# Performance work log

Hardware: AMD Instinct MI355X
Metric: run time of the kernel (lower is better)

Reference implementation:

```python
import jax, jax.numpy as jnp
import numpy as np

D_MODEL = 1024
N_HEAD = 16
HEAD_DIM = D_MODEL // N_HEAD


def setup_inputs() -> dict:
    key = jax.random.key(0)
    ks = jax.random.split(key, 9)
    B, S, D = 2, 2048, D_MODEL
    s = 1.0 / np.sqrt(D)
    return {
        "x": jax.random.normal(ks[0], (B, S, D), dtype=jnp.float32),
        "Wq": jax.random.normal(ks[1], (D, D), dtype=jnp.float32) * s,
        "bq": jnp.zeros((D,), dtype=jnp.float32),
        "Wk": jax.random.normal(ks[2], (D, D), dtype=jnp.float32) * s,
        "bk": jnp.zeros((D,), dtype=jnp.float32),
        "Wv": jax.random.normal(ks[3], (D, D), dtype=jnp.float32) * s,
        "bv": jnp.zeros((D,), dtype=jnp.float32),
        "Wo": jax.random.normal(ks[4], (D, D), dtype=jnp.float32) * s,
        "bo": jnp.zeros((D,), dtype=jnp.float32),
    }


def _split_heads(t):
    B, S, D = t.shape
    return t.reshape(B, S, N_HEAD, HEAD_DIM).transpose(0, 2, 1, 3)  # [B,H,S,d]


def reference(x, Wq, bq, Wk, bk, Wv, bv, Wo, bo):
    B, S, D = x.shape
    q = _split_heads(x @ Wq + bq)
    k = _split_heads(x @ Wk + bk)
    v = _split_heads(x @ Wv + bv)
    present = jnp.stack((k, v))  # [2,B,H,S,d]
    # NOTE: module scales by sqrt(d_model), not sqrt(head_dim)
    scores = jnp.einsum("bhqd,bhkd->bhqk", q, k) / jnp.sqrt(jnp.float32(D_MODEL))
    causal = jnp.tril(jnp.ones((S, S), dtype=bool))
    scores = jnp.where(causal, scores, -jnp.inf)
    probs = jax.nn.softmax(scores, axis=-1)
    attn = jnp.einsum("bhqk,bhkd->bhqd", probs, v)
    attn = attn.transpose(0, 2, 1, 3).reshape(B, S, D)
    out = attn @ Wo + bo
    return out, present
```

## Files before the change

kernel.cpp:

```cpp
#include <hip/hip_runtime.h>
#include <hip/hip_bf16.h>

typedef __attribute__((ext_vector_type(8))) short short8;
typedef __attribute__((ext_vector_type(4))) short short4v;
typedef __attribute__((ext_vector_type(4))) float f32x4;

#define S_LEN 2048
#define DM 1024
#define NH 16
#define HD 64

__device__ __forceinline__ short f2b(float f) {
    __hip_bfloat16 h = __float2bfloat16(f);
    return *reinterpret_cast<short*>(&h);
}

__global__ void k_convert_x(const float* __restrict__ x, short* __restrict__ xb) {
    size_t i = ((size_t)blockIdx.x * blockDim.x + threadIdx.x) * 4;
    f32x4 v = *reinterpret_cast<const f32x4*>(x + i);
    short4v o;
    for (int e = 0; e < 4; e++) o[e] = f2b(v[e]);
    *reinterpret_cast<short4v*>(xb + i) = o;
}

__global__ void k_transpose_w4(const float* __restrict__ W0, const float* __restrict__ W1,
                               const float* __restrict__ W2, const float* __restrict__ W3,
                               short* __restrict__ T0, short* __restrict__ T1,
                               short* __restrict__ T2, short* __restrict__ T3) {
    __shared__ float tile[32][33];
    const int z = blockIdx.z;
    const float* W = (z == 0) ? W0 : (z == 1) ? W1 : (z == 2) ? W2 : W3;
    short* Wt = (z == 0) ? T0 : (z == 1) ? T1 : (z == 2) ? T2 : T3;
    int tx = threadIdx.x, ty = threadIdx.y;
    int nb = blockIdx.x * 32, kb = blockIdx.y * 32;
    for (int i = 0; i < 4; i++)
        tile[ty + i * 8][tx] = W[(size_t)(kb + ty + i * 8) * DM + nb + tx];
    __syncthreads();
    for (int i = 0; i < 4; i++)
        Wt[(size_t)(nb + ty + i * 8) * DM + kb + tx] = f2b(tile[tx][ty + i * 8]);
}

__global__ __launch_bounds__(256) void k_gemm_qkv(
    const short* __restrict__ xb,
    const short* __restrict__ Wqt, const short* __restrict__ Wkt, const short* __restrict__ Wvt,
    const float* __restrict__ bq, const float* __restrict__ bk, const float* __restrict__ bv,
    short* __restrict__ Qb, short* __restrict__ Kfrag, short* __restrict__ Vfrag,
    float* __restrict__ pK, float* __restrict__ pV)
{
    __shared__ alignas(16) short As[128][72];
    __shared__ alignas(16) short Bs[128][72];
    const int z = blockIdx.z;
    const short* Wt  = (z == 0) ? Wqt : (z == 1) ? Wkt : Wvt;
    const float* bias = (z == 0) ? bq : (z == 1) ? bk : bv;
    const int t = threadIdx.x;
    const int brow = blockIdx.y * 128, bcol = blockIdx.x * 128;
    const int w = t >> 6, l = t & 63;
    const int wr = w >> 1, wc = w & 1;
    const int lr = l & 15, lg = l >> 4;
    f32x4 acc[4][4];
    for (int m = 0; m < 4; m++) for (int n = 0; n < 4; n++) acc[m][n] = (f32x4)0.0f;

    for (int k0 = 0; k0 < DM; k0 += 64) {
        __syncthreads();
        for (int i = 0; i < 4; i++) {
            int idx = i * 256 + t;
            int r = idx >> 3, c8 = (idx & 7) * 8;
            *reinterpret_cast<short8*>(&As[r][c8]) =
                *reinterpret_cast<const short8*>(&xb[(size_t)(brow + r) * DM + k0 + c8]);
            *reinterpret_cast<short8*>(&Bs[r][c8]) =
                *reinterpret_cast<const short8*>(&Wt[(size_t)(bcol + r) * DM + k0 + c8]);
        }
        __syncthreads();
        for (int ks = 0; ks < 2; ks++) {
            short8 a[4], bb[4];
            const int kk = ks * 32 + lg * 8;
            for (int m = 0; m < 4; m++)
                a[m] = *reinterpret_cast<const short8*>(&As[wr * 64 + m * 16 + lr][kk]);
            for (int n = 0; n < 4; n++)
                bb[n] = *reinterpret_cast<const short8*>(&Bs[wc * 64 + n * 16 + lr][kk]);
            for (int m = 0; m < 4; m++)
                for (int n = 0; n < 4; n++)
                    acc[m][n] = __builtin_amdgcn_mfma_f32_16x16x32_bf16(a[m], bb[n], acc[m][n], 0, 0, 0);
        }
    }
    for (int m = 0; m < 4; m++)
        for (int n = 0; n < 4; n++) {
            int row = brow + wr * 64 + m * 16 + lg * 4;
            int col = bcol + wc * 64 + n * 16 + lr;
            float bv_ = bias[col];
            int b_ = row >> 11, sI0 = row & 2047, hI = col >> 6, dh = col & 63;
            if (z == 0) {
                for (int r = 0; r < 4; r++) {
                    float v = acc[m][n][r] + bv_;
                    Qb[(size_t)(row + r) * DM + col] = f2b(v * 0.0450842200575152f);
                }
            } else if (z == 1) {
                for (int r = 0; r < 4; r++) {
                    float v = acc[m][n][r] + bv_;
                    int sI = sI0 + r;
                    pK[(((size_t)(b_ * NH + hI)) * S_LEN + sI) * HD + dh] = v;
                    int j = sI >> 6, kk = sI & 63;
                    int cg = ((kk >> 4) & 2) | ((kk >> 2) & 1);
                    int lrA = ((kk >> 3) & 3) * 4 + (kk & 3);
                    int lane = lrA + ((dh >> 3) & 3) * 16;
                    int ks = dh >> 5, e = dh & 7;
                    Kfrag[((((size_t)(b_ * NH + hI) * 32 + j) * 2 + ks) * 4 + cg) * 512
                          + lane * 8 + e] = f2b(v);
                }
            } else {
                int j = sI0 >> 6, ks = (sI0 >> 5) & 1;
                int dg = dh >> 4;
                int lane = (dh & 15) + ((sI0 >> 3) & 3) * 16;
                int e0 = sI0 & 7;
                short4v tv;
                for (int r = 0; r < 4; r++) {
                    float v = acc[m][n][r] + bv_;
                    pV[(((size_t)(b_ * NH + hI)) * S_LEN + (sI0 + r)) * HD + dh] = v;
                    tv[r] = f2b(v);
                }
                *reinterpret_cast<short4v*>(
                    &Vfrag[((((size_t)(b_ * NH + hI) * 32 + j) * 2 + ks) * 4 + dg) * 512
                           + lane * 8 + e0]) = tv;
            }
        }
}

__global__ __launch_bounds__(256) void k_gemm_o(
    const short* __restrict__ Ab, const short* __restrict__ Wot,
    const float* __restrict__ bo, float* __restrict__ out)
{
    __shared__ alignas(16) short As[128][72];
    __shared__ alignas(16) short Bs[128][72];
    const int t = threadIdx.x;
    const int brow = blockIdx.y * 128, bcol = blockIdx.x * 128;
    const int w = t >> 6, l = t & 63;
    const int wr = w >> 1, wc = w & 1;
    const int lr = l & 15, lg = l >> 4;
    f32x4 acc[4][4];
    for (int m = 0; m < 4; m++) for (int n = 0; n < 4; n++) acc[m][n] = (f32x4)0.0f;

    for (int k0 = 0; k0 < DM; k0 += 64) {
        __syncthreads();
        for (int i = 0; i < 4; i++) {
            int idx = i * 256 + t;
            int r = idx >> 3, c8 = (idx & 7) * 8;
            *reinterpret_cast<short8*>(&As[r][c8]) =
                *reinterpret_cast<const short8*>(&Ab[(size_t)(brow + r) * DM + k0 + c8]);
            *reinterpret_cast<short8*>(&Bs[r][c8]) =
                *reinterpret_cast<const short8*>(&Wot[(size_t)(bcol + r) * DM + k0 + c8]);
        }
        __syncthreads();
        for (int ks = 0; ks < 2; ks++) {
            short8 a[4], bb[4];
            const int kk = ks * 32 + lg * 8;
            for (int m = 0; m < 4; m++)
                a[m] = *reinterpret_cast<const short8*>(&As[wr * 64 + m * 16 + lr][kk]);
            for (int n = 0; n < 4; n++)
                bb[n] = *reinterpret_cast<const short8*>(&Bs[wc * 64 + n * 16 + lr][kk]);
            for (int m = 0; m < 4; m++)
                for (int n = 0; n < 4; n++)
                    acc[m][n] = __builtin_amdgcn_mfma_f32_16x16x32_bf16(a[m], bb[n], acc[m][n], 0, 0, 0);
        }
    }
    for (int m = 0; m < 4; m++)
        for (int n = 0; n < 4; n++) {
            int row = brow + wr * 64 + m * 16 + lg * 4;
            int col = bcol + wc * 64 + n * 16 + lr;
            float bv_ = bo[col];
            for (int r = 0; r < 4; r++)
                out[(size_t)(row + r) * DM + col] = acc[m][n][r] + bv_;
        }
}

__global__ __launch_bounds__(64) void k_attn(
    const short* __restrict__ Qb, const short* __restrict__ Kfrag,
    const short* __restrict__ Vfrag, short* __restrict__ Ab)
{
    const int bid = blockIdx.x;
    const int orig = (bid & 7) * 256 + (bid >> 3);
    const int bh = orig >> 6, rp = orig & 63;
    const int h = bh & 15, b = bh >> 4;
    const int l = threadIdx.x;
    const int lr = l & 15, lg = l >> 4;
    const size_t base = (size_t)b * S_LEN * DM + (size_t)h * HD;
    const short* Qp = Qb + base;
    const short* Kbh = Kfrag + (size_t)bh * 32 * 4096;
    const short* Vbh = Vfrag + (size_t)bh * 32 * 4096;
    short* Ap = Ab + base;

    for (int phase = 0; phase < 2; ++phase) {
        const int strip = phase ? 127 - rp : rp;
        const int jmax = strip >> 2;
        const int qrow = strip * 16 + lr;
        short8 qf0 = *reinterpret_cast<const short8*>(Qp + (size_t)qrow * DM + lg * 8);
        short8 qf1 = *reinterpret_cast<const short8*>(Qp + (size_t)qrow * DM + 32 + lg * 8);
        f32x4 o[4];
#pragma unroll
        for (int dg = 0; dg < 4; dg++) o[dg] = (f32x4)0.0f;
        float mrun = -INFINITY, lrun = 0.0f;

        const short* kp = Kbh + l * 8;
        const short* vp = Vbh + l * 8;
        short8 kc[2][4], vc[2][4];
#pragma unroll
        for (int ks = 0; ks < 2; ks++)
#pragma unroll
            for (int cg = 0; cg < 4; cg++) {
                kc[ks][cg] = *reinterpret_cast<const short8*>(kp + (ks * 4 + cg) * 512);
                vc[ks][cg] = *reinterpret_cast<const short8*>(vp + (ks * 4 + cg) * 512);
            }

        for (int j = 0; j <= jmax; ++j) {
            f32x4 s[4];
#pragma unroll
            for (int cg = 0; cg < 4; cg++) s[cg] = (f32x4)0.0f;
#pragma unroll
            for (int ks = 0; ks < 2; ks++) {
                const short8 qf = ks ? qf1 : qf0;
#pragma unroll
                for (int cg = 0; cg < 4; cg++)
                    s[cg] = __builtin_amdgcn_mfma_f32_16x16x32_bf16(kc[ks][cg], qf, s[cg], 0, 0, 0);
            }
            if (j < jmax) {
                kp += 4096;
#pragma unroll
                for (int ks = 0; ks < 2; ks++)
#pragma unroll
                    for (int cg = 0; cg < 4; cg++)
                        kc[ks][cg] = *reinterpret_cast<const short8*>(kp + (ks * 4 + cg) * 512);
            }
            if (j == jmax) {
#pragma unroll
                for (int cg = 0; cg < 4; cg++)
#pragma unroll
                    for (int r = 0; r < 4; r++) {
                        int n = ((cg >> 1) << 5) + (lg << 3) + ((cg & 1) << 2) + r;
                        if (j * 64 + n > qrow) s[cg][r] = -INFINITY;
                    }
            }
            float mx0 = fmaxf(fmaxf(s[0][0], s[0][1]), fmaxf(s[0][2], s[0][3]));
            float mx1 = fmaxf(fmaxf(s[1][0], s[1][1]), fmaxf(s[1][2], s[1][3]));
            float mx2 = fmaxf(fmaxf(s[2][0], s[2][1]), fmaxf(s[2][2], s[2][3]));
            float mx3 = fmaxf(fmaxf(s[3][0], s[3][1]), fmaxf(s[3][2], s[3][3]));
            float vmax = fmaxf(fmaxf(mx0, mx1), fmaxf(mx2, mx3));
            vmax = fmaxf(vmax, __shfl_xor(vmax, 16));
            vmax = fmaxf(vmax, __shfl_xor(vmax, 32));
            if (!__all(vmax - mrun <= 8.0f)) {
                float mn = fmaxf(mrun, vmax);
                float scl = exp2f(mrun - mn);
                mrun = mn; lrun *= scl;
#pragma unroll
                for (int dg = 0; dg < 4; dg++)
#pragma unroll
                    for (int r = 0; r < 4; r++) o[dg][r] *= scl;
            }
            float rs = 0.0f;
#pragma unroll
            for (int cg = 0; cg < 4; cg++)
#pragma unroll
                for (int r = 0; r < 4; r++) {
                    float p = exp2f(s[cg][r] - mrun);
                    s[cg][r] = p;
                    rs += p;
                }
            rs += __shfl_xor(rs, 16);
            rs += __shfl_xor(rs, 32);
            lrun += rs;
            short8 pf0, pf1;
#pragma unroll
            for (int r = 0; r < 4; r++) {
                pf0[r] = f2b(s[0][r]); pf0[4 + r] = f2b(s[1][r]);
                pf1[r] = f2b(s[2][r]); pf1[4 + r] = f2b(s[3][r]);
            }
#pragma unroll
            for (int ks = 0; ks < 2; ks++) {
                const short8 pf = ks ? pf1 : pf0;
#pragma unroll
                for (int dg = 0; dg < 4; dg++)
                    o[dg] = __builtin_amdgcn_mfma_f32_16x16x32_bf16(vc[ks][dg], pf, o[dg], 0, 0, 0);
            }
            if (j < jmax) {
                vp += 4096;
#pragma unroll
                for (int ks = 0; ks < 2; ks++)
#pragma unroll
                    for (int cg = 0; cg < 4; cg++)
                        vc[ks][cg] = *reinterpret_cast<const short8*>(vp + (ks * 4 + cg) * 512);
            }
        }
        float rinv = 1.0f / lrun;
#pragma unroll
        for (int dg = 0; dg < 4; dg++) {
            short4v ov;
#pragma unroll
            for (int r = 0; r < 4; r++) ov[r] = f2b(o[dg][r] * rinv);
            *reinterpret_cast<short4v*>(Ap + (size_t)qrow * DM + dg * 16 + lg * 4) = ov;
        }
    }
}

extern "C" void kernel_launch(void* const* d_in, const int* in_sizes, int n_in,
                              void* d_out, int out_size, void* d_ws, size_t ws_size,
                              hipStream_t stream) {
    const float* x  = (const float*)d_in[0];
    const float* Wq = (const float*)d_in[1];
    const float* bq = (const float*)d_in[2];
    const float* Wk = (const float*)d_in[3];
    const float* bk = (const float*)d_in[4];
    const float* Wv = (const float*)d_in[5];
    const float* bv = (const float*)d_in[6];
    const float* Wo = (const float*)d_in[7];
    const float* bo = (const float*)d_in[8];

    float* out = (float*)d_out;
    float* presentK = out + (size_t)4194304;
    float* presentV = presentK + (size_t)4194304;

    char* ws = (char*)d_ws;
    short* xb    = (short*)(ws);
    short* Wqt   = (short*)(ws + ((size_t)8  << 20));
    short* Wkt   = (short*)(ws + ((size_t)10 << 20));
    short* Wvt   = (short*)(ws + ((size_t)12 << 20));
    short* Wot   = (short*)(ws + ((size_t)14 << 20));
    short* Qb    = (short*)(ws + ((size_t)16 << 20));
    short* Kfrag = (short*)(ws + ((size_t)24 << 20));
    short* Vfrag = (short*)(ws + ((size_t)32 << 20));
    short* Ab    = (short*)(ws + ((size_t)40 << 20));

    k_convert_x<<<dim3(4096), dim3(256), 0, stream>>>(x, xb);
    k_transpose_w4<<<dim3(32, 32, 4), dim3(32, 8), 0, stream>>>(
        Wq, Wk, Wv, Wo, Wqt, Wkt, Wvt, Wot);
    k_gemm_qkv<<<dim3(8, 32, 3), dim3(256), 0, stream>>>(
        xb, Wqt, Wkt, Wvt, bq, bk, bv, Qb, Kfrag, Vfrag, presentK, presentV);
    k_attn<<<dim3(2048), dim3(64), 0, stream>>>(Qb, Kfrag, Vfrag, Ab);
    k_gemm_o<<<dim3(8, 32), dim3(256), 0, stream>>>(Ab, Wot, bo, out);
}
```

Baseline: 140.9 us.

## Process two query strips per wave sharing K/V fragments, two waves per block

Each wave now handles two adjacent 16-row query strips (A and B) against the same K/V fragment loads, halving K/V global traffic per query row. The former sequential two-phase causal balancing becomes two waves per block, each taking a mirrored strip pair, and the grid halves to 1024 blocks of 128 threads. In exchange, register pressure roughly doubles for accumulators and scores, which may reduce occupancy, and there are fewer blocks in flight.

```diff
diff --git a/kernel.cpp b/kernel.cpp
--- a/kernel.cpp
+++ b/kernel.cpp
@@ -172,15 +172,15 @@
         }
 }
 
-__global__ __launch_bounds__(64) void k_attn(
+__global__ __launch_bounds__(128) void k_attn(
     const short* __restrict__ Qb, const short* __restrict__ Kfrag,
     const short* __restrict__ Vfrag, short* __restrict__ Ab)
 {
     const int bid = blockIdx.x;
-    const int orig = (bid & 7) * 256 + (bid >> 3);
-    const int bh = orig >> 6, rp = orig & 63;
+    const int orig = (bid & 7) * 128 + (bid >> 3);
+    const int bh = orig >> 5, kidx = orig & 31;
     const int h = bh & 15, b = bh >> 4;
-    const int l = threadIdx.x;
+    const int w = threadIdx.x >> 6, l = threadIdx.x & 63;
     const int lr = l & 15, lg = l >> 4;
     const size_t base = (size_t)b * S_LEN * DM + (size_t)h * HD;
     const short* Qp = Qb + base;
@@ -188,114 +188,166 @@
     const short* Vbh = Vfrag + (size_t)bh * 32 * 4096;
     short* Ap = Ab + base;
 
-    for (int phase = 0; phase < 2; ++phase) {
-        const int strip = phase ? 127 - rp : rp;
-        const int jmax = strip >> 2;
-        const int qrow = strip * 16 + lr;
-        short8 qf0 = *reinterpret_cast<const short8*>(Qp + (size_t)qrow * DM + lg * 8);
-        short8 qf1 = *reinterpret_cast<const short8*>(Qp + (size_t)qrow * DM + 32 + lg * 8);
-        f32x4 o[4];
-#pragma unroll
-        for (int dg = 0; dg < 4; dg++) o[dg] = (f32x4)0.0f;
-        float mrun = -INFINITY, lrun = 0.0f;
-
-        const short* kp = Kbh + l * 8;
-        const short* vp = Vbh + l * 8;
-        short8 kc[2][4], vc[2][4];
-#pragma unroll
-        for (int ks = 0; ks < 2; ks++)
+    const int kj = w ? 63 - kidx : kidx;
+    const int jmax = kj >> 1;
+    const int qrowA = (2 * kj) * 16 + lr;
+    const int qrowB = (2 * kj + 1) * 16 + lr;
+
+    short8 qfA0 = *reinterpret_cast<const short8*>(Qp + (size_t)qrowA * DM + lg * 8);
+    short8 qfA1 = *reinterpret_cast<const short8*>(Qp + (size_t)qrowA * DM + 32 + lg * 8);
+    short8 qfB0 = *reinterpret_cast<const short8*>(Qp + (size_t)qrowB * DM + lg * 8);
+    short8 qfB1 = *reinterpret_cast<const short8*>(Qp + (size_t)qrowB * DM + 32 + lg * 8);
+    f32x4 oA[4], oB[4];
+#pragma unroll
+    for (int dg = 0; dg < 4; dg++) { oA[dg] = (f32x4)0.0f; oB[dg] = (f32x4)0.0f; }
+    float mrunA = -INFINITY, lrunA = 0.0f;
+    float mrunB = -INFINITY, lrunB = 0.0f;
+
+    const short* kp = Kbh + l * 8;
+    const short* vp = Vbh + l * 8;
+    short8 kc[2][4], vc[2][4];
+#pragma unroll
+    for (int ks = 0; ks < 2; ks++)
+#pragma unroll
+        for (int cg = 0; cg < 4; cg++) {
+            kc[ks][cg] = *reinterpret_cast<const short8*>(kp + (ks * 4 + cg) * 512);
+            vc[ks][cg] = *reinterpret_cast<const short8*>(vp + (ks * 4 + cg) * 512);
+        }
+
+    for (int j = 0; j <= jmax; ++j) {
+        f32x4 sA[4], sB[4];
+#pragma unroll
+        for (int cg = 0; cg < 4; cg++) { sA[cg] = (f32x4)0.0f; sB[cg] = (f32x4)0.0f; }
+#pragma unroll
+        for (int ks = 0; ks < 2; ks++) {
+            const short8 qfa = ks ? qfA1 : qfA0;
+            const short8 qfb = ks ? qfB1 : qfB0;
 #pragma unroll
             for (int cg = 0; cg < 4; cg++) {
-                kc[ks][cg] = *reinterpret_cast<const short8*>(kp + (ks * 4 + cg) * 512);
-                vc[ks][cg] = *reinterpret_cast<const short8*>(vp + (ks * 4 + cg) * 512);
-            }
-
-        for (int j = 0; j <= jmax; ++j) {
-            f32x4 s[4];
-#pragma unroll
-            for (int cg = 0; cg < 4; cg++) s[cg] = (f32x4)0.0f;
-#pragma unroll
-            for (int ks = 0; ks < 2; ks++) {
-                const short8 qf = ks ? qf1 : qf0;
+                sA[cg] = __builtin_amdgcn_mfma_f32_16x16x32_bf16(kc[ks][cg], qfa, sA[cg], 0, 0, 0);
+                sB[cg] = __builtin_amdgcn_mfma_f32_16x16x32_bf16(kc[ks][cg], qfb, sB[cg], 0, 0, 0);
+            }
+        }
+        if (j < jmax) {
+            kp += 4096;
+#pragma unroll
+            for (int ks = 0; ks < 2; ks++)
 #pragma unroll
                 for (int cg = 0; cg < 4; cg++)
-                    s[cg] = __builtin_amdgcn_mfma_f32_16x16x32_bf16(kc[ks][cg], qf, s[cg], 0, 0, 0);
-            }
-            if (j < jmax) {
-                kp += 4096;
-#pragma unroll
-                for (int ks = 0; ks < 2; ks++)
-#pragma unroll
-                    for (int cg = 0; cg < 4; cg++)
-                        kc[ks][cg] = *reinterpret_cast<const short8*>(kp + (ks * 4 + cg) * 512);
-            }
-            if (j == jmax) {
-#pragma unroll
-                for (int cg = 0; cg < 4; cg++)
-#pragma unroll
-                    for (int r = 0; r < 4; r++) {
-                        int n = ((cg >> 1) << 5) + (lg << 3) + ((cg & 1) << 2) + r;
-                        if (j * 64 + n > qrow) s[cg][r] = -INFINITY;
-                    }
-            }
-            float mx0 = fmaxf(fmaxf(s[0][0], s[0][1]), fmaxf(s[0][2], s[0][3]));
-            float mx1 = fmaxf(fmaxf(s[1][0], s[1][1]), fmaxf(s[1][2], s[1][3]));
-            float mx2 = fmaxf(fmaxf(s[2][0], s[2][1]), fmaxf(s[2][2], s[2][3]));
-            float mx3 = fmaxf(fmaxf(s[3][0], s[3][1]), fmaxf(s[3][2], s[3][3]));
+                    kc[ks][cg] = *reinterpret_cast<const short8*>(kp + (ks * 4 + cg) * 512);
+        }
+        if (j == jmax) {
+#pragma unroll
+            for (int cg = 0; cg < 4; cg++)
+#pragma unroll
+                for (int r = 0; r < 4; r++) {
+                    int n = ((cg >> 1) << 5) + (lg << 3) + ((cg & 1) << 2) + r;
+                    if (j * 64 + n > qrowA) sA[cg][r] = -INFINITY;
+                    if (j * 64 + n > qrowB) sB[cg][r] = -INFINITY;
+                }
+        }
+        short8 pfA0, pfA1;
+        {
+            float mx0 = fmaxf(fmaxf(sA[0][0], sA[0][1]), fmaxf(sA[0][2], sA[0][3]));
+            float mx1 = fmaxf(fmaxf(sA[1][0], sA[1][1]), fmaxf(sA[1][2], sA[1][3]));
+            float mx2 = fmaxf(fmaxf(sA[2][0], sA[2][1]), fmaxf(sA[2][2], sA[2][3]));
+            float mx3 = fmaxf(fmaxf(sA[3][0], sA[3][1]), fmaxf(sA[3][2], sA[3][3]));
             float vmax = fmaxf(fmaxf(mx0, mx1), fmaxf(mx2, mx3));
             vmax = fmaxf(vmax, __shfl_xor(vmax, 16));
             vmax = fmaxf(vmax, __shfl_xor(vmax, 32));
-            if (!__all(vmax - mrun <= 8.0f)) {
-                float mn = fmaxf(mrun, vmax);
-                float scl = exp2f(mrun - mn);
-                mrun = mn; lrun *= scl;
+            if (!__all(vmax - mrunA <= 8.0f)) {
+                float mn = fmaxf(mrunA, vmax);
+                float scl = exp2f(mrunA - mn);
+                mrunA = mn; lrunA *= scl;
 #pragma unroll
                 for (int dg = 0; dg < 4; dg++)
 #pragma unroll
-                    for (int r = 0; r < 4; r++) o[dg][r] *= scl;
+                    for (int r = 0; r < 4; r++) oA[dg][r] *= scl;
             }
             float rs = 0.0f;
 #pragma unroll
             for (int cg = 0; cg < 4; cg++)
 #pragma unroll
                 for (int r = 0; r < 4; r++) {
-                    float p = exp2f(s[cg][r] - mrun);
-                    s[cg][r] = p;
+                    float p = exp2f(sA[cg][r] - mrunA);
+                    sA[cg][r] = p;
                     rs += p;
                 }
             rs += __shfl_xor(rs, 16);
             rs += __shfl_xor(rs, 32);
-            lrun += rs;
-            short8 pf0, pf1;
+            lrunA += rs;
 #pragma unroll
             for (int r = 0; r < 4; r++) {
-                pf0[r] = f2b(s[0][r]); pf0[4 + r] = f2b(s[1][r]);
-                pf1[r] = f2b(s[2][r]); pf1[4 + r] = f2b(s[3][r]);
-            }
-#pragma unroll
-            for (int ks = 0; ks < 2; ks++) {
-                const short8 pf = ks ? pf1 : pf0;
+                pfA0[r] = f2b(sA[0][r]); pfA0[4 + r] = f2b(sA[1][r]);
+                pfA1[r] = f2b(sA[2][r]); pfA1[4 + r] = f2b(sA[3][r]);
+            }
+        }
+        short8 pfB0, pfB1;
+        {
+            float mx0 = fmaxf(fmaxf(sB[0][0], sB[0][1]), fmaxf(sB[0][2], sB[0][3]));
+            float mx1 = fmaxf(fmaxf(sB[1][0], sB[1][1]), fmaxf(sB[1][2], sB[1][3]));
+            float mx2 = fmaxf(fmaxf(sB[2][0], sB[2][1]), fmaxf(sB[2][2], sB[2][3]));
+            float mx3 = fmaxf(fmaxf(sB[3][0], sB[3][1]), fmaxf(sB[3][2], sB[3][3]));
+            float vmax = fmaxf(fmaxf(mx0, mx1), fmaxf(mx2, mx3));
+            vmax = fmaxf(vmax, __shfl_xor(vmax, 16));
+            vmax = fmaxf(vmax, __shfl_xor(vmax, 32));
+            if (!__all(vmax - mrunB <= 8.0f)) {
+                float mn = fmaxf(mrunB, vmax);
+                float scl = exp2f(mrunB - mn);
+                mrunB = mn; lrunB *= scl;
 #pragma unroll
                 for (int dg = 0; dg < 4; dg++)
-                    o[dg] = __builtin_amdgcn_mfma_f32_16x16x32_bf16(vc[ks][dg], pf, o[dg], 0, 0, 0);
-            }
-            if (j < jmax) {
-                vp += 4096;
-#pragma unroll
-                for (int ks = 0; ks < 2; ks++)
-#pragma unroll
-                    for (int cg = 0; cg < 4; cg++)
-                        vc[ks][cg] = *reinterpret_cast<const short8*>(vp + (ks * 4 + cg) * 512);
-            }
-        }
-        float rinv = 1.0f / lrun;
-#pragma unroll
-        for (int dg = 0; dg < 4; dg++) {
-            short4v ov;
-#pragma unroll
-            for (int r = 0; r < 4; r++) ov[r] = f2b(o[dg][r] * rinv);
-            *reinterpret_cast<short4v*>(Ap + (size_t)qrow * DM + dg * 16 + lg * 4) = ov;
-        }
+#pragma unroll
+                    for (int r = 0; r < 4; r++) oB[dg][r] *= scl;
+            }
+            float rs = 0.0f;
+#pragma unroll
+            for (int cg = 0; cg < 4; cg++)
+#pragma unroll
+                for (int r = 0; r < 4; r++) {
+                    float p = exp2f(sB[cg][r] - mrunB);
+                    sB[cg][r] = p;
+                    rs += p;
+                }
+            rs += __shfl_xor(rs, 16);
+            rs += __shfl_xor(rs, 32);
+            lrunB += rs;
+#pragma unroll
+            for (int r = 0; r < 4; r++) {
+                pfB0[r] = f2b(sB[0][r]); pfB0[4 + r] = f2b(sB[1][r]);
+                pfB1[r] = f2b(sB[2][r]); pfB1[4 + r] = f2b(sB[3][r]);
+            }
+        }
+#pragma unroll
+        for (int ks = 0; ks < 2; ks++) {
+            const short8 pfa = ks ? pfA1 : pfA0;
+            const short8 pfb = ks ? pfB1 : pfB0;
+#pragma unroll
+            for (int dg = 0; dg < 4; dg++) {
+                oA[dg] = __builtin_amdgcn_mfma_f32_16x16x32_bf16(vc[ks][dg], pfa, oA[dg], 0, 0, 0);
+                oB[dg] = __builtin_amdgcn_mfma_f32_16x16x32_bf16(vc[ks][dg], pfb, oB[dg], 0, 0, 0);
+            }
+        }
+        if (j < jmax) {
+            vp += 4096;
+#pragma unroll
+            for (int ks = 0; ks < 2; ks++)
+#pragma unroll
+                for (int cg = 0; cg < 4; cg++)
+                    vc[ks][cg] = *reinterpret_cast<const short8*>(vp + (ks * 4 + cg) * 512);
+        }
+    }
+    float rinvA = 1.0f / lrunA, rinvB = 1.0f / lrunB;
+#pragma unroll
+    for (int dg = 0; dg < 4; dg++) {
+        short4v ovA, ovB;
+#pragma unroll
+        for (int r = 0; r < 4; r++) {
+            ovA[r] = f2b(oA[dg][r] * rinvA);
+            ovB[r] = f2b(oB[dg][r] * rinvB);
+        }
+        *reinterpret_cast<short4v*>(Ap + (size_t)qrowA * DM + dg * 16 + lg * 4) = ovA;
+        *reinterpret_cast<short4v*>(Ap + (size_t)qrowB * DM + dg * 16 + lg * 4) = ovB;
     }
 }
 
@@ -332,6 +384,6 @@
         Wq, Wk, Wv, Wo, Wqt, Wkt, Wvt, Wot);
     k_gemm_qkv<<<dim3(8, 32, 3), dim3(256), 0, stream>>>(
         xb, Wqt, Wkt, Wvt, bq, bk, bv, Qb, Kfrag, Vfrag, presentK, presentV);
-    k_attn<<<dim3(2048), dim3(64), 0, stream>>>(Qb, Kfrag, Vfrag, Ab);
+    k_attn<<<dim3(1024), dim3(128), 0, stream>>>(Qb, Kfrag, Vfrag, Ab);
     k_gemm_o<<<dim3(8, 32), dim3(256), 0, stream>>>(Ab, Wot, bo, out);
 }
```

Result: slower. 147.1 us (+4.4%).

## Pre-swizzle QKV GEMM operands into MFMA fragment layout and drop LDS staging

Applied to the files above, without the earlier changes.

The x conversion and Wq/Wk/Wv transpose kernels now write bf16 data directly in the per-lane MFMA fragment order. The QKV GEMM then becomes a single-wave-per-block kernel that loads fragments straight from global memory with no shared-memory staging or barriers. Block IDs are remapped so that neighbouring blocks are spread across XCDs. This removes the LDS round trip and the synchronisation, but each wave now rereads A and B from global memory or L2 with no reuse across waves, and there is no software prefetching.

```diff
diff --git a/kernel.cpp b/kernel.cpp
--- a/kernel.cpp
+++ b/kernel.cpp
@@ -15,12 +15,18 @@
     return *reinterpret_cast<short*>(&h);
 }
 
-__global__ void k_convert_x(const float* __restrict__ x, short* __restrict__ xb) {
-    size_t i = ((size_t)blockIdx.x * blockDim.x + threadIdx.x) * 4;
-    f32x4 v = *reinterpret_cast<const f32x4*>(x + i);
-    short4v o;
-    for (int e = 0; e < 4; e++) o[e] = f2b(v[e]);
-    *reinterpret_cast<short4v*>(xb + i) = o;
+__global__ void k_convert_x(const float* __restrict__ x, short* __restrict__ Af) {
+    int t = blockIdx.x * 256 + threadIdx.x;
+    int s = t >> 7, kc = t & 127;
+    const float* xp = x + (size_t)s * DM + kc * 8;
+    f32x4 v0 = *reinterpret_cast<const f32x4*>(xp);
+    f32x4 v1 = *reinterpret_cast<const f32x4*>(xp + 4);
+    short8 o;
+    for (int e = 0; e < 4; e++) { o[e] = f2b(v0[e]); o[4 + e] = f2b(v1[e]); }
+    int R = s >> 6, m = (s >> 4) & 3, lr = s & 15;
+    int kstep = kc >> 3, ks = (kc >> 2) & 1, lg = kc & 3;
+    size_t off = ((((size_t)(R * 16 + kstep) * 2 + ks) * 4 + m) * 64 + lg * 16 + lr) * 8;
+    *reinterpret_cast<short8*>(Af + off) = o;
 }
 
 __global__ void k_transpose_w4(const float* __restrict__ W0, const float* __restrict__ W1,
@@ -36,57 +42,69 @@
     for (int i = 0; i < 4; i++)
         tile[ty + i * 8][tx] = W[(size_t)(kb + ty + i * 8) * DM + nb + tx];
     __syncthreads();
-    for (int i = 0; i < 4; i++)
-        Wt[(size_t)(nb + ty + i * 8) * DM + kb + tx] = f2b(tile[tx][ty + i * 8]);
-}
-
-__global__ __launch_bounds__(256) void k_gemm_qkv(
-    const short* __restrict__ xb,
-    const short* __restrict__ Wqt, const short* __restrict__ Wkt, const short* __restrict__ Wvt,
+    for (int i = 0; i < 4; i++) {
+        int col = nb + ty + i * 8, k = kb + tx;
+        short val = f2b(tile[tx][ty + i * 8]);
+        if (z == 3) {
+            Wt[(size_t)col * DM + k] = val;
+        } else {
+            int C = col >> 6, n = (col >> 4) & 3, lr = col & 15;
+            int kstep = k >> 6, ksb = (k >> 5) & 1, lg = (k >> 3) & 3, e = k & 7;
+            Wt[((((size_t)(C * 16 + kstep) * 2 + ksb) * 4 + n) * 64 + lg * 16 + lr) * 8 + e] = val;
+        }
+    }
+}
+
+__global__ __launch_bounds__(64) void k_gemm_qkv(
+    const short* __restrict__ Af,
+    const short* __restrict__ Bq, const short* __restrict__ Bk, const short* __restrict__ Bv,
     const float* __restrict__ bq, const float* __restrict__ bk, const float* __restrict__ bv,
     short* __restrict__ Qb, short* __restrict__ Kfrag, short* __restrict__ Vfrag,
     float* __restrict__ pK, float* __restrict__ pV)
 {
-    __shared__ alignas(16) short As[128][72];
-    __shared__ alignas(16) short Bs[128][72];
-    const int z = blockIdx.z;
-    const short* Wt  = (z == 0) ? Wqt : (z == 1) ? Wkt : Wvt;
+    const int bid = blockIdx.x;
+    const unsigned orig = (bid & 7) * 384 + (bid >> 3);
+    const int R = orig / 48;
+    const int rem = orig - R * 48;
+    const int z = rem >> 4, C = rem & 15;
+    const short* Bf = (z == 0) ? Bq : (z == 1) ? Bk : Bv;
     const float* bias = (z == 0) ? bq : (z == 1) ? bk : bv;
-    const int t = threadIdx.x;
-    const int brow = blockIdx.y * 128, bcol = blockIdx.x * 128;
-    const int w = t >> 6, l = t & 63;
-    const int wr = w >> 1, wc = w & 1;
+    const int l = threadIdx.x;
     const int lr = l & 15, lg = l >> 4;
+
     f32x4 acc[4][4];
-    for (int m = 0; m < 4; m++) for (int n = 0; n < 4; n++) acc[m][n] = (f32x4)0.0f;
-
-    for (int k0 = 0; k0 < DM; k0 += 64) {
-        __syncthreads();
-        for (int i = 0; i < 4; i++) {
-            int idx = i * 256 + t;
-            int r = idx >> 3, c8 = (idx & 7) * 8;
-            *reinterpret_cast<short8*>(&As[r][c8]) =
-                *reinterpret_cast<const short8*>(&xb[(size_t)(brow + r) * DM + k0 + c8]);
-            *reinterpret_cast<short8*>(&Bs[r][c8]) =
-                *reinterpret_cast<const short8*>(&Wt[(size_t)(bcol + r) * DM + k0 + c8]);
-        }
-        __syncthreads();
-        for (int ks = 0; ks < 2; ks++) {
-            short8 a[4], bb[4];
-            const int kk = ks * 32 + lg * 8;
+#pragma unroll
+    for (int m = 0; m < 4; m++)
+#pragma unroll
+        for (int n = 0; n < 4; n++) acc[m][n] = (f32x4)0.0f;
+
+    const short* ap = Af + (size_t)R * 16 * 4096 + l * 8;
+    const short* bp = Bf + (size_t)C * 16 * 4096 + l * 8;
+
+#pragma unroll 1
+    for (int kstep = 0; kstep < 16; ++kstep) {
+        short8 a[2][4], b[2][4];
+#pragma unroll
+        for (int ks = 0; ks < 2; ks++)
+#pragma unroll
+            for (int i = 0; i < 4; i++) {
+                a[ks][i] = *reinterpret_cast<const short8*>(ap + (ks * 4 + i) * 512);
+                b[ks][i] = *reinterpret_cast<const short8*>(bp + (ks * 4 + i) * 512);
+            }
+        ap += 4096; bp += 4096;
+#pragma unroll
+        for (int ks = 0; ks < 2; ks++)
+#pragma unroll
             for (int m = 0; m < 4; m++)
-                a[m] = *reinterpret_cast<const short8*>(&As[wr * 64 + m * 16 + lr][kk]);
-            for (int n = 0; n < 4; n++)
-                bb[n] = *reinterpret_cast<const short8*>(&Bs[wc * 64 + n * 16 + lr][kk]);
-            for (int m = 0; m < 4; m++)
+#pragma unroll
                 for (int n = 0; n < 4; n++)
-                    acc[m][n] = __builtin_amdgcn_mfma_f32_16x16x32_bf16(a[m], bb[n], acc[m][n], 0, 0, 0);
-        }
+                    acc[m][n] = __builtin_amdgcn_mfma_f32_16x16x32_bf16(a[ks][m], b[ks][n], acc[m][n], 0, 0, 0);
     }
+
     for (int m = 0; m < 4; m++)
         for (int n = 0; n < 4; n++) {
-            int row = brow + wr * 64 + m * 16 + lg * 4;
-            int col = bcol + wc * 64 + n * 16 + lr;
+            int row = R * 64 + m * 16 + lg * 4;
+            int col = C * 64 + n * 16 + lr;
             float bv_ = bias[col];
             int b_ = row >> 11, sI0 = row & 2047, hI = col >> 6, dh = col & 63;
             if (z == 0) {
@@ -317,21 +335,21 @@
     float* presentV = presentK + (size_t)4194304;
 
     char* ws = (char*)d_ws;
-    short* xb    = (short*)(ws);
-    short* Wqt   = (short*)(ws + ((size_t)8  << 20));
-    short* Wkt   = (short*)(ws + ((size_t)10 << 20));
-    short* Wvt   = (short*)(ws + ((size_t)12 << 20));
+    short* Af    = (short*)(ws);
+    short* Bfq   = (short*)(ws + ((size_t)8  << 20));
+    short* Bfk   = (short*)(ws + ((size_t)10 << 20));
+    short* Bfv   = (short*)(ws + ((size_t)12 << 20));
     short* Wot   = (short*)(ws + ((size_t)14 << 20));
     short* Qb    = (short*)(ws + ((size_t)16 << 20));
     short* Kfrag = (short*)(ws + ((size_t)24 << 20));
     short* Vfrag = (short*)(ws + ((size_t)32 << 20));
     short* Ab    = (short*)(ws + ((size_t)40 << 20));
 
-    k_convert_x<<<dim3(4096), dim3(256), 0, stream>>>(x, xb);
+    k_convert_x<<<dim3(2048), dim3(256), 0, stream>>>(x, Af);
     k_transpose_w4<<<dim3(32, 32, 4), dim3(32, 8), 0, stream>>>(
-        Wq, Wk, Wv, Wo, Wqt, Wkt, Wvt, Wot);
-    k_gemm_qkv<<<dim3(8, 32, 3), dim3(256), 0, stream>>>(
-        xb, Wqt, Wkt, Wvt, bq, bk, bv, Qb, Kfrag, Vfrag, presentK, presentV);
+        Wq, Wk, Wv, Wo, Bfq, Bfk, Bfv, Wot);
+    k_gemm_qkv<<<dim3(3072), dim3(64), 0, stream>>>(
+        Af, Bfq, Bfk, Bfv, bq, bk, bv, Qb, Kfrag, Vfrag, presentK, presentV);
     k_attn<<<dim3(2048), dim3(64), 0, stream>>>(Qb, Kfrag, Vfrag, Ab);
     k_gemm_o<<<dim3(8, 32), dim3(256), 0, stream>>>(Ab, Wot, bo, out);
 }
```

Result: faster. 123.3 us (-12.5%).
